# Performance work log

Hardware: AMD Instinct MI355X
Metric: run time of the kernel (lower is better)

The kernel has to match this reference:

```python
import jax, jax.numpy as jnp
import numpy as np

TEMP = 0.07
BASE_TEMP = 0.07
EPS = 1e-12


def setup_inputs() -> dict:
    key = jax.random.key(0)
    k1, k2, k3 = jax.random.split(key, 3)
    B, V, D, C = 4096, 1, 128, 100
    features = jax.random.normal(k1, (B, V, D), dtype=jnp.float32)
    labels = jax.random.randint(k2, (B,), 0, C, dtype=jnp.int64)
    covariances = jax.random.normal(k3, (C, D, D), dtype=jnp.float32)
    return {"features": features, "labels": labels, "covariances": covariances}


def reference(features, labels, covariances):
    B, n_views = features.shape[0], features.shape[1]
    feats = features.reshape(B, n_views, -1)
    # cat(unbind(dim=1), dim=0); with n_views==1 this is feats[:, 0]
    contrast_feature = jnp.concatenate([feats[:, v] for v in range(n_views)], axis=0)
    anchor_feature = contrast_feature  # contrast_mode == 'all'

    # mask_{i,j} = 1 if labels match
    mask = (labels[:, None] == labels[None, :]).astype(jnp.float32)  # [B,B]

    similarity_matrix = anchor_feature @ contrast_feature.T  # [B,B]

    # dis[i,j] = a_i^T C_{label_i} a_j  (gather cov per anchor, one bilinear form per pair)
    cov_g = covariances[labels]                              # [B,D,D] irregular gather
    v = jnp.einsum('id,ide->ie', anchor_feature, cov_g)      # [B,D]
    dis_matrix = v @ anchor_feature.T                        # [B,B]

    logits = (similarity_matrix + dis_matrix / (2.0 * TEMP ** 2)) / TEMP
    logits = logits - jax.lax.stop_gradient(jnp.max(logits, axis=1, keepdims=True))
    log_prob = logits - jnp.log(jnp.sum(jnp.exp(logits), axis=1, keepdims=True) + EPS)

    # original: (mask[:,:,None] * log_prob).sum(1) == mask @ log_prob (avoids B^3 temp)
    mask_sum = mask.sum(axis=1, keepdims=True)               # [B,1]
    mean_log_prob_pos = (mask @ log_prob) / (mask_sum + EPS)  # [B,B]
    loss = -(TEMP / BASE_TEMP) * mean_log_prob_pos
    return loss.mean()
```

## Files before the change

kernel.cpp:

```cpp
#include <hip/hip_runtime.h>
#include <hip/hip_bf16.h>


#define DIM 128
#define TEMP 0.07f
#define PITCH 136

typedef __attribute__((ext_vector_type(8))) short short8;
typedef __attribute__((ext_vector_type(4))) float floatx4;

static __device__ __forceinline__ unsigned short f2bf(float f) {
    __hip_bfloat16 h = __float2bfloat16(f);
    union { __hip_bfloat16 h; unsigned short u; } c;
    c.h = h;
    return c.u;
}

__global__ __launch_bounds__(256) void conv_kernel(
    const float* __restrict__ A, unsigned short* __restrict__ O, int n) {
    int i = (blockIdx.x * 256 + threadIdx.x) * 4;
    if (i < n) {
        float4 v = *(const float4*)(A + i);
        ushort4 o;
        o.x = f2bf(v.x); o.y = f2bf(v.y); o.z = f2bf(v.z); o.w = f2bf(v.w);
        *(ushort4*)(O + i) = o;
    }
}

__global__ __launch_bounds__(128) void w_kernel(
    const float* __restrict__ A, const int* __restrict__ labels,
    const float* __restrict__ Cov, unsigned short* __restrict__ Wbf) {
    const float inv2t2 = 1.0f / (2.0f * TEMP * TEMP);
    const float invt = 1.0f / TEMP;
    int i = blockIdx.x;
    int e = threadIdx.x;
    __shared__ float a[DIM];
    a[e] = A[(size_t)i * DIM + e];
    __syncthreads();
    int c = labels[i];
    const float* Cp = Cov + (size_t)c * (DIM * DIM) + e;
    float acc = 0.0f;
#pragma unroll 8
    for (int d = 0; d < DIM; ++d) {
        acc = fmaf(a[d], Cp[(size_t)d * DIM], acc);
    }
    Wbf[(size_t)i * DIM + e] = f2bf((a[e] + acc * inv2t2) * invt);
}

__global__ __launch_bounds__(256, 2) void main_kernel(
    const unsigned short* __restrict__ Wbf, const unsigned short* __restrict__ Abf,
    float* __restrict__ mP, float* __restrict__ zP, float* __restrict__ sP,
    int Jsplit, int JSWEEP, int nP) {
    __shared__ __align__(16) unsigned short sW[128 * PITCH];
    __shared__ __align__(16) unsigned short sA[64 * PITCH];

    const int mb = blockIdx.x / Jsplit;
    const int jsp = blockIdx.x % Jsplit;
    const int rowBase = mb * 128;
    const int t = threadIdx.x;
    const int wave = t >> 6, lane = t & 63, quad = lane >> 4, l16 = lane & 15;
    const int waveM = wave >> 1, waveN = wave & 1;

    {
        int row = t >> 1, half = t & 1;
        const unsigned short* src = Wbf + (size_t)(rowBase + row) * DIM + half * 64;
        unsigned short* dst = sW + row * PITCH + half * 64;
#pragma unroll
        for (int i = 0; i < 8; i++)
            *(short8*)(dst + i * 8) = *(const short8*)(src + i * 8);
    }

    float run_m[4][4], run_Z[4][4], run_s[4][4];
#pragma unroll
    for (int a = 0; a < 4; a++)
#pragma unroll
        for (int r = 0; r < 4; r++) {
            run_m[a][r] = -3.4e38f; run_Z[a][r] = 0.f; run_s[a][r] = 0.f;
        }

    const unsigned short* myW = sW + (waveM * 64 + l16) * PITCH;
    const unsigned short* myA = sA + (waveN * 32 + l16) * PITCH;

    for (int js = 0; js < JSWEEP; ++js) {
        __syncthreads();
        {
            int row = t >> 2, q = t & 3;
            int j0 = (jsp * JSWEEP + js) * 64;
            const unsigned short* src = Abf + (size_t)(j0 + row) * DIM + q * 32;
            unsigned short* dst = sA + row * PITCH + q * 32;
#pragma unroll
            for (int i = 0; i < 4; i++)
                *(short8*)(dst + i * 8) = *(const short8*)(src + i * 8);
        }
        __syncthreads();

        floatx4 acc[4][2];
#pragma unroll
        for (int mt = 0; mt < 4; mt++)
#pragma unroll
            for (int nt = 0; nt < 2; nt++) acc[mt][nt] = (floatx4)0.f;

#pragma unroll
        for (int kst = 0; kst < 4; ++kst) {
            const int koff = kst * 32 + quad * 8;
            short8 bfrag[2];
#pragma unroll
            for (int nt = 0; nt < 2; nt++)
                bfrag[nt] = *(const short8*)(myA + nt * 16 * PITCH + koff);
#pragma unroll
            for (int mt = 0; mt < 4; mt++) {
                short8 afrag = *(const short8*)(myW + mt * 16 * PITCH + koff);
#pragma unroll
                for (int nt = 0; nt < 2; nt++)
                    acc[mt][nt] = __builtin_amdgcn_mfma_f32_16x16x32_bf16(
                        afrag, bfrag[nt], acc[mt][nt], 0, 0, 0);
            }
        }

#pragma unroll
        for (int mt = 0; mt < 4; mt++)
#pragma unroll
            for (int r = 0; r < 4; r++) {
                float v0 = acc[mt][0][r], v1 = acc[mt][1][r];
                float tm = fmaxf(v0, v1);
                float nm = fmaxf(run_m[mt][r], tm);
                run_Z[mt][r] = run_Z[mt][r] * __expf(run_m[mt][r] - nm)
                             + __expf(v0 - nm) + __expf(v1 - nm);
                run_m[mt][r] = nm;
                run_s[mt][r] += v0 + v1;
            }
    }

    const int chunk = jsp * 2 + waveN;
#pragma unroll
    for (int mt = 0; mt < 4; mt++)
#pragma unroll
        for (int r = 0; r < 4; r++) {
            float m = run_m[mt][r], Z = run_Z[mt][r], s = run_s[mt][r];
#pragma unroll
            for (int mask = 1; mask < 16; mask <<= 1) {
                float om = __shfl_xor(m, mask);
                float oZ = __shfl_xor(Z, mask);
                float os = __shfl_xor(s, mask);
                float nm = fmaxf(m, om);
                Z = Z * __expf(m - nm) + oZ * __expf(om - nm);
                m = nm;
                s += os;
            }
            if (l16 == r) {
                int row = rowBase + waveM * 64 + mt * 16 + quad * 4 + r;
                size_t idx = (size_t)row * nP + chunk;
                mP[idx] = m; zP[idx] = Z; sP[idx] = s;
            }
        }
}

__global__ __launch_bounds__(64) void combine_kernel(
    const float* __restrict__ mP, const float* __restrict__ zP,
    const float* __restrict__ sP, const int* __restrict__ labels,
    double* __restrict__ G, int* __restrict__ counts, int B, int nP) {
    int k = blockIdx.x;
    int l = threadIdx.x;
    float m = -3.4e38f, Z = 0.0f, s = 0.0f;
    if (l < nP) {
        size_t idx = (size_t)k * nP + l;
        m = mP[idx]; Z = zP[idx]; s = sP[idx];
    }
    float M = m;
#pragma unroll
    for (int o = 32; o > 0; o >>= 1) M = fmaxf(M, __shfl_xor(M, o));
    float zt = Z * __expf(m - M);
    float st = s;
#pragma unroll
    for (int o = 32; o > 0; o >>= 1) {
        zt += __shfl_xor(zt, o);
        st += __shfl_xor(st, o);
    }
    if (l == 0) {
        double Sk = (double)st - (double)B * (double)M
                    - (double)B * log((double)zt + 1e-12);
        int c = labels[k];
        atomicAdd(&G[c], Sk);
        atomicAdd(&counts[c], 1);
    }
}

__global__ __launch_bounds__(128) void final_kernel(
    const double* __restrict__ G, const int* __restrict__ counts,
    float* __restrict__ out, int C, double invB2) {
    __shared__ double sh[128];
    int t = threadIdx.x;
    double v = 0.0;
    if (t < C) {
        double cnt = (double)counts[t];
        v = G[t] * (cnt / (cnt + 1e-12));
    }
    sh[t] = v;
    __syncthreads();
    for (int o = 64; o > 0; o >>= 1) {
        if (t < o) sh[t] += sh[t + o];
        __syncthreads();
    }
    if (t == 0) out[0] = (float)(-sh[0] * invB2);
}

extern "C" void kernel_launch(void* const* d_in, const int* in_sizes, int n_in,
                              void* d_out, int out_size, void* d_ws, size_t ws_size,
                              hipStream_t stream) {
    const float* A = (const float*)d_in[0];
    const int* labels = (const int*)d_in[1];
    const float* Cov = (const float*)d_in[2];
    float* out = (float*)d_out;

    int B = in_sizes[0] / DIM;
    int C = in_sizes[2] / (DIM * DIM);
    int Jsplit = 16;
    int JSWEEP = B / (Jsplit * 64);
    int nP = Jsplit * 2;

    char* ws = (char*)d_ws;
    unsigned short* Wbf = (unsigned short*)ws;
    unsigned short* Abf = Wbf + (size_t)B * DIM;
    float* mP = (float*)(Abf + (size_t)B * DIM);
    float* zP = mP + (size_t)B * nP;
    float* sP = zP + (size_t)B * nP;
    double* G = (double*)(sP + (size_t)B * nP);
    int* counts = (int*)(G + C);

    hipMemsetAsync(G, 0, (size_t)C * (sizeof(double) + sizeof(int)), stream);

    int nA = B * DIM;
    conv_kernel<<<(nA / 4 + 255) / 256, 256, 0, stream>>>(A, Abf, nA);
    w_kernel<<<B, 128, 0, stream>>>(A, labels, Cov, Wbf);
    main_kernel<<<(B / 128) * Jsplit, 256, 0, stream>>>(Wbf, Abf, mP, zP, sP,
                                                        Jsplit, JSWEEP, nP);
    combine_kernel<<<B, 64, 0, stream>>>(mP, zP, sP, labels, G, counts, B, nP);
    final_kernel<<<1, 128, 0, stream>>>(G, counts, out, C,
                                        1.0 / ((double)B * (double)B));
}
```

Measured before the change: 114.2 us.

## Fuse prep kernels and fold combine/final reductions into main kernel via tickets

Merges the bf16 conversion, the W computation and the zeroing of the accumulators into a single prep kernel, which removes the memset and one launch. The per-row combine and the final reduction move into the tail of main_kernel, using atomic ticket counters so the last block per row-block and the last block overall do that work. This cuts the pipeline from six GPU operations to two, trading launch overhead for threadfence and atomic synchronisation and a serial tail in the last block. The partial results are now stored chunk-major so the combine reads are coalesced.

Measured after the change: 184.3 us. 1.61x slower.

```diff
diff --git a/kernel.cpp b/kernel.cpp
--- a/kernel.cpp
+++ b/kernel.cpp
@@ -16,43 +16,46 @@
     return c.u;
 }
 
-__global__ __launch_bounds__(256) void conv_kernel(
-    const float* __restrict__ A, unsigned short* __restrict__ O, int n) {
-    int i = (blockIdx.x * 256 + threadIdx.x) * 4;
-    if (i < n) {
-        float4 v = *(const float4*)(A + i);
-        ushort4 o;
-        o.x = f2bf(v.x); o.y = f2bf(v.y); o.z = f2bf(v.z); o.w = f2bf(v.w);
-        *(ushort4*)(O + i) = o;
-    }
-}
-
-__global__ __launch_bounds__(128) void w_kernel(
+__global__ __launch_bounds__(256) void prep_kernel(
     const float* __restrict__ A, const int* __restrict__ labels,
-    const float* __restrict__ Cov, unsigned short* __restrict__ Wbf) {
+    const float* __restrict__ Cov, unsigned short* __restrict__ Wbf,
+    unsigned short* __restrict__ Abf, double* __restrict__ G,
+    int* __restrict__ counts, int* __restrict__ tickets, int C) {
     const float inv2t2 = 1.0f / (2.0f * TEMP * TEMP);
     const float invt = 1.0f / TEMP;
-    int i = blockIdx.x;
-    int e = threadIdx.x;
-    __shared__ float a[DIM];
-    a[e] = A[(size_t)i * DIM + e];
+    const int sub = threadIdx.x >> 7;
+    const int e = threadIdx.x & 127;
+    const int i = blockIdx.x * 2 + sub;
+    __shared__ float a[2][DIM];
+    float av = A[(size_t)i * DIM + e];
+    a[sub][e] = av;
+    Abf[(size_t)i * DIM + e] = f2bf(av);
+    if (blockIdx.x == 0) {
+        int t = threadIdx.x;
+        if (t < C) { G[t] = 0.0; counts[t] = 0; }
+        if (t >= 128 && t < 128 + 33) tickets[t - 128] = 0;
+    }
     __syncthreads();
     int c = labels[i];
     const float* Cp = Cov + (size_t)c * (DIM * DIM) + e;
     float acc = 0.0f;
 #pragma unroll 8
     for (int d = 0; d < DIM; ++d) {
-        acc = fmaf(a[d], Cp[(size_t)d * DIM], acc);
-    }
-    Wbf[(size_t)i * DIM + e] = f2bf((a[e] + acc * inv2t2) * invt);
+        acc = fmaf(a[sub][d], Cp[(size_t)d * DIM], acc);
+    }
+    Wbf[(size_t)i * DIM + e] = f2bf((av + acc * inv2t2) * invt);
 }
 
 __global__ __launch_bounds__(256, 2) void main_kernel(
     const unsigned short* __restrict__ Wbf, const unsigned short* __restrict__ Abf,
+    const int* __restrict__ labels,
     float* __restrict__ mP, float* __restrict__ zP, float* __restrict__ sP,
-    int Jsplit, int JSWEEP, int nP) {
+    double* __restrict__ G, int* __restrict__ counts, int* __restrict__ tickets,
+    float* __restrict__ out, int B, int Jsplit, int JSWEEP, int nP, int C) {
     __shared__ __align__(16) unsigned short sW[128 * PITCH];
     __shared__ __align__(16) unsigned short sA[64 * PITCH];
+    __shared__ int flag;
+    __shared__ double sh[256];
 
     const int mb = blockIdx.x / Jsplit;
     const int jsp = blockIdx.x % Jsplit;
@@ -149,59 +152,57 @@
             }
             if (l16 == r) {
                 int row = rowBase + waveM * 64 + mt * 16 + quad * 4 + r;
-                size_t idx = (size_t)row * nP + chunk;
+                size_t idx = (size_t)chunk * B + row;
                 mP[idx] = m; zP[idx] = Z; sP[idx] = s;
             }
         }
-}
-
-__global__ __launch_bounds__(64) void combine_kernel(
-    const float* __restrict__ mP, const float* __restrict__ zP,
-    const float* __restrict__ sP, const int* __restrict__ labels,
-    double* __restrict__ G, int* __restrict__ counts, int B, int nP) {
-    int k = blockIdx.x;
-    int l = threadIdx.x;
-    float m = -3.4e38f, Z = 0.0f, s = 0.0f;
-    if (l < nP) {
-        size_t idx = (size_t)k * nP + l;
-        m = mP[idx]; Z = zP[idx]; s = sP[idx];
-    }
-    float M = m;
-#pragma unroll
-    for (int o = 32; o > 0; o >>= 1) M = fmaxf(M, __shfl_xor(M, o));
-    float zt = Z * __expf(m - M);
-    float st = s;
-#pragma unroll
-    for (int o = 32; o > 0; o >>= 1) {
-        zt += __shfl_xor(zt, o);
-        st += __shfl_xor(st, o);
-    }
-    if (l == 0) {
-        double Sk = (double)st - (double)B * (double)M
-                    - (double)B * log((double)zt + 1e-12);
-        int c = labels[k];
-        atomicAdd(&G[c], Sk);
-        atomicAdd(&counts[c], 1);
-    }
-}
-
-__global__ __launch_bounds__(128) void final_kernel(
-    const double* __restrict__ G, const int* __restrict__ counts,
-    float* __restrict__ out, int C, double invB2) {
-    __shared__ double sh[128];
-    int t = threadIdx.x;
-    double v = 0.0;
-    if (t < C) {
-        double cnt = (double)counts[t];
-        v = G[t] * (cnt / (cnt + 1e-12));
-    }
-    sh[t] = v;
-    __syncthreads();
-    for (int o = 64; o > 0; o >>= 1) {
-        if (t < o) sh[t] += sh[t + o];
+
+    __threadfence();
+    __syncthreads();
+    if (t == 0) flag = (atomicAdd(&tickets[mb], 1) == Jsplit - 1);
+    __syncthreads();
+    if (flag) {
+        __threadfence();
+        if (t < 128) {
+            int k = rowBase + t;
+            float m = -3.4e38f, Z = 0.f, s = 0.f;
+            for (int p = 0; p < nP; ++p) {
+                size_t idx = (size_t)p * B + k;
+                float mi = mP[idx];
+                float nm = fmaxf(m, mi);
+                Z = Z * __expf(m - nm) + zP[idx] * __expf(mi - nm);
+                m = nm;
+                s += sP[idx];
+            }
+            double Sk = (double)s - (double)B * (double)m
+                        - (double)B * log((double)Z + 1e-12);
+            int c = labels[k];
+            atomicAdd(&G[c], Sk);
+            atomicAdd(&counts[c], 1);
+        }
+    }
+
+    __threadfence();
+    __syncthreads();
+    if (t == 0) flag = (atomicAdd(&tickets[32], 1) == (int)gridDim.x - 1);
+    __syncthreads();
+    if (flag) {
+        __threadfence();
+        double v = 0.0;
+        if (t < C) {
+            double g = atomicAdd(&G[t], 0.0);
+            double cnt = (double)atomicAdd(&counts[t], 0);
+            v = g * (cnt / (cnt + 1e-12));
+        }
+        sh[t] = v;
         __syncthreads();
-    }
-    if (t == 0) out[0] = (float)(-sh[0] * invB2);
+        for (int o = 128; o > 0; o >>= 1) {
+            if (t < o) sh[t] += sh[t + o];
+            __syncthreads();
+        }
+        if (t == 0)
+            out[0] = (float)(-sh[0] / ((double)B * (double)B));
+    }
 }
 
 extern "C" void kernel_launch(void* const* d_in, const int* in_sizes, int n_in,
@@ -226,15 +227,11 @@
     float* sP = zP + (size_t)B * nP;
     double* G = (double*)(sP + (size_t)B * nP);
     int* counts = (int*)(G + C);
-
-    hipMemsetAsync(G, 0, (size_t)C * (sizeof(double) + sizeof(int)), stream);
-
-    int nA = B * DIM;
-    conv_kernel<<<(nA / 4 + 255) / 256, 256, 0, stream>>>(A, Abf, nA);
-    w_kernel<<<B, 128, 0, stream>>>(A, labels, Cov, Wbf);
-    main_kernel<<<(B / 128) * Jsplit, 256, 0, stream>>>(Wbf, Abf, mP, zP, sP,
-                                                        Jsplit, JSWEEP, nP);
-    combine_kernel<<<B, 64, 0, stream>>>(mP, zP, sP, labels, G, counts, B, nP);
-    final_kernel<<<1, 128, 0, stream>>>(G, counts, out, C,
-                                        1.0 / ((double)B * (double)B));
-}
+    int* tickets = counts + C;
+
+    prep_kernel<<<B / 2, 256, 0, stream>>>(A, labels, Cov, Wbf, Abf,
+                                           G, counts, tickets, C);
+    main_kernel<<<(B / 128) * Jsplit, 256, 0, stream>>>(
+        Wbf, Abf, labels, mP, zP, sP, G, counts, tickets, out,
+        B, Jsplit, JSWEEP, nP, C);
+}
```
